# Optimization experiments

Hardware: AMD Instinct MI355X
Metric: run time of the kernel (lower is better)

Reference implementation:

```python
import jax, jax.numpy as jnp
import numpy as np
from jax import lax

NUM_PATHS = 16384
NUM_EDGES = 4096
LINK_DIM = 128   # link_state_dim (GRU input dim)
PATH_DIM = 128   # path_state_dim (GRU units)
MAX_LEN = 20     # max path length (static scatter shape)


def setup_inputs() -> dict:
    key = jax.random.key(0)
    ks = jax.random.split(key, 8)
    rng = np.random.default_rng(0)
    lens_np = rng.integers(4, MAX_LEN + 1, size=NUM_PATHS)
    lens_np[0] = MAX_LEN  # ensure max_len is reached
    total = int(lens_np.sum())
    idx_np = np.repeat(np.arange(NUM_PATHS), lens_np)
    offsets = np.repeat(np.concatenate([[0], np.cumsum(lens_np)[:-1]]), lens_np)
    seqs_np = np.arange(total) - offsets
    paths_np = rng.integers(0, NUM_EDGES, size=total)
    scale = 0.05
    return {
        "inputs": jax.random.normal(ks[0], (NUM_EDGES, LINK_DIM), jnp.float32),
        "paths": jnp.asarray(paths_np, jnp.int32),
        "idx": jnp.asarray(idx_np, jnp.int32),
        "seqs": jnp.asarray(seqs_np, jnp.int32),
        "lens": jnp.asarray(lens_np, jnp.int32),
        "gru_kernel": jax.random.normal(ks[1], (LINK_DIM, 3 * PATH_DIM), jnp.float32) * scale,
        "gru_rkernel": jax.random.normal(ks[2], (PATH_DIM, 3 * PATH_DIM), jnp.float32) * scale,
        "gru_bias": jax.random.normal(ks[3], (2, 3 * PATH_DIM), jnp.float32) * scale,
        "wq": jax.random.normal(ks[4], (PATH_DIM, PATH_DIM), jnp.float32) * scale,
        "wk": jax.random.normal(ks[5], (PATH_DIM, PATH_DIM), jnp.float32) * scale,
        "wv": jax.random.normal(ks[6], (PATH_DIM, PATH_DIM), jnp.float32) * scale,
    }


def _pem_forward(inputs, paths, idx, seqs, lens, gru_kernel, gru_rkernel, gru_bias, wq, wk, wv):
    P = lens.shape[0]
    D = gru_rkernel.shape[0]
    # gather per-step edge states and pack into padded [P, L, Din] sequences
    h_tild = inputs[paths]                                        # [T, Din]
    link_inputs = jnp.zeros((P, MAX_LEN, inputs.shape[1]), inputs.dtype)
    link_inputs = link_inputs.at[idx, seqs].set(h_tild)

    mask = jnp.arange(MAX_LEN, dtype=lens.dtype)[:, None] < lens[None, :]  # [L, P]
    xs = jnp.swapaxes(link_inputs, 0, 1)                          # [L, P, Din]

    def step(h, inp):
        x, m = inp
        xz, xr, xh = jnp.split(x @ gru_kernel + gru_bias[0], 3, axis=-1)
        hz, hr, hh = jnp.split(h @ gru_rkernel + gru_bias[1], 3, axis=-1)
        z = jax.nn.sigmoid(xz + hz)
        r = jax.nn.sigmoid(xr + hr)
        cand = jnp.tanh(xh + r * hh)
        h_new = z * h + (1.0 - z) * cand
        m2 = m[:, None]
        h_next = jnp.where(m2, h_new, h)        # carry state past sequence end
        y = jnp.where(m2, h_new, 0.0)           # zero outputs past sequence end
        return h_next, y

    h0 = jnp.zeros((P, D), inputs.dtype)
    last_state, hs = lax.scan(step, h0, (xs, mask))
    hidden_states = jnp.swapaxes(hs, 0, 1)                        # [P, L, D]

    key_ = jnp.einsum('pld,de->ple', hidden_states, wk)
    query = last_state @ wq                                       # [P, D]
    value = jnp.einsum('pld,de->ple', hidden_states, wv)
    att = jnp.einsum('pld,pd->pl', key_, query)                   # no softmax (as in source)
    context = jnp.einsum('pl,pld->pd', att, value)[:, None, :]    # [P, 1, D]
    return context


def reference(inputs, paths, idx, seqs, lens, gru_kernel, gru_rkernel, gru_bias, wq, wk, wv):
    return _pem_forward(inputs, paths, idx, seqs, lens,
                        gru_kernel, gru_rkernel, gru_bias, wq, wk, wv)
```

## Files before the change

### kernel.cpp

```cpp
#include <hip/hip_runtime.h>
#include <cstdint>

#define NP 16384
#define NE 4096
#define DIM 128
#define ML 20
#define TP 32
#define NT (NP/TP)

typedef _Float16 f16;
typedef _Float16 f16x8 __attribute__((ext_vector_type(8)));
typedef _Float16 f16x2 __attribute__((ext_vector_type(2)));
typedef float    f32x4 __attribute__((ext_vector_type(4)));

__global__ __launch_bounds__(1024) void k_sort(const int* __restrict__ lens,
                                               int* __restrict__ perm) {
    __shared__ int wcnt[16][33];
    __shared__ int start[ML + 1];
    const int tid = threadIdx.x;
    const int wv  = tid >> 6;
    for (int i = tid; i < 16 * 33; i += 1024) ((int*)wcnt)[i] = 0;
    __syncthreads();
    #pragma unroll
    for (int k = 0; k < NP / 1024; ++k) {
        const int p = k * 1024 + tid;
        atomicAdd(&wcnt[wv][lens[p]], 1);
    }
    __syncthreads();
    if (tid == 0) {
        int s = 0;
        for (int i = ML; i >= 0; --i) {
            int c = 0;
            #pragma unroll
            for (int w2 = 0; w2 < 16; ++w2) c += wcnt[w2][i];
            start[i] = s; s += c;
        }
    }
    __syncthreads();
    if (tid <= ML) {
        int running = start[tid];
        #pragma unroll
        for (int w2 = 0; w2 < 16; ++w2) {
            int tmp = wcnt[w2][tid];
            wcnt[w2][tid] = running;
            running += tmp;
        }
    }
    __syncthreads();
    #pragma unroll
    for (int k = 0; k < NP / 1024; ++k) {
        const int p = k * 1024 + tid;
        int pos = atomicAdd(&wcnt[wv][lens[p]], 1);
        perm[pos] = p;
    }
}

__global__ void k_prep(const int* __restrict__ idx, const int* __restrict__ seqs,
                       const int* __restrict__ paths, int total,
                       const float* __restrict__ inputs,
                       const float* __restrict__ gk, const float* __restrict__ gr,
                       int* __restrict__ edge_map, f16* __restrict__ inx,
                       f16* __restrict__ btz, f16* __restrict__ btr,
                       f16* __restrict__ btcx, f16* __restrict__ btch) {
    const int i = blockIdx.x * 256 + threadIdx.x;
    if (i < total) edge_map[idx[i] * ML + seqs[i]] = paths[i];
    inx[i] = (f16)inputs[i];
    if (i < 16384) {
        const int n = i >> 7, k = i & 127;
        btz[n*256 + k]       = (f16)gk[k*384 + n];
        btz[n*256 + 128 + k] = (f16)gr[k*384 + n];
        btr[n*256 + k]       = (f16)gk[k*384 + 128 + n];
        btr[n*256 + 128 + k] = (f16)gr[k*384 + 128 + n];
        btcx[n*128 + k]      = (f16)gk[k*384 + 256 + n];
        btch[n*128 + k]      = (f16)gr[k*384 + 256 + n];
    }
}

__device__ __forceinline__ float frcp(float x)  { return __builtin_amdgcn_rcpf(x); }
__device__ __forceinline__ float fsig(float x)  { return frcp(1.f + __expf(-x)); }
__device__ __forceinline__ float ftanh(float x) { float e = __expf(2.f * x); return 1.f - 2.f * frcp(e + 1.f); }


__global__ __launch_bounds__(512, 2) void k_gru(
    const f16* __restrict__ inx, const int* __restrict__ lens,
    const f16* __restrict__ btz, const f16* __restrict__ btr,
    const f16* __restrict__ btcx, const f16* __restrict__ btch,
    const float* __restrict__ gb, const int* __restrict__ edge_map,
    const int* __restrict__ perm, f16* __restrict__ hs, float* __restrict__ last)
{
    __shared__ f16 H16[2][TP * DIM];
    __shared__ int pgs[TP], lns[TP];

    const int tid  = threadIdx.x;
    const int lane = tid & 63;
    const int w    = tid >> 6;
    const int nw   = w * 16;
    const int arow = lane & 15;
    const int agrp = lane >> 4;
    const int d    = nw + arow;

    if (tid < TP) { int pg = perm[blockIdx.x * TP + tid]; pgs[tid] = pg; lns[tid] = lens[pg]; }
    for (int i = tid; i < TP * DIM; i += 512) H16[0][i] = (f16)0.f;
    asm volatile("s_waitcnt lgkmcnt(0)" ::: "memory");
    __builtin_amdgcn_s_barrier();

    int tmax = 0;
    #pragma unroll
    for (int i = 0; i < TP; ++i) tmax = max(tmax, lns[i]);

    f16x8 Bz[8], Br[8], Bx[4], Bh[4];
    {
        const int cb = d * 256 + agrp * 8;
        #pragma unroll
        for (int ks = 0; ks < 8; ++ks) {
            Bz[ks] = *(const f16x8*)(btz + cb + ks * 32);
            Br[ks] = *(const f16x8*)(btr + cb + ks * 32);
        }
        const int cc = d * 128 + agrp * 8;
        #pragma unroll
        for (int ks = 0; ks < 4; ++ks) {
            Bx[ks] = *(const f16x8*)(btcx + cc + ks * 32);
            Bh[ks] = *(const f16x8*)(btch + cc + ks * 32);
        }
    }

    const float bzc = gb[d]       + gb[384 + d];
    const float brc = gb[128 + d] + gb[512 + d];
    const float bxc = gb[256 + d];
    const float bhc = gb[640 + d];

    float hold0[4] = {0.f,0.f,0.f,0.f}, hold1[4] = {0.f,0.f,0.f,0.f};
    int ln0[4], ln1[4], hsr0[4], hsr1[4], h16a0[4], h16a1[4], pg0[4], pg1[4];
    #pragma unroll
    for (int r = 0; r < 4; ++r) {
        const int pa = agrp * 4 + r;
        const int pb = 16 + pa;
        ln0[r] = lns[pa];            ln1[r] = lns[pb];
        pg0[r] = pgs[pa];            pg1[r] = pgs[pb];
        hsr0[r] = pgs[pa] * ML;      hsr1[r] = pgs[pb] * ML;
        h16a0[r] = pa * DIM + (((d >> 3) ^ (pa & 7)) * 8) + (d & 7);
        h16a1[r] = pb * DIM + (((d >> 3) ^ (pb & 7)) * 8) + (d & 7);
    }

    const int ep0 = pgs[arow] * ML;
    const int ep1 = pgs[16 + arow] * ML;

    f16x8 xa0[4], xa1[4];
    int en0, en1;
    {
        const int e0 = edge_map[ep0] & (NE - 1);
        const int e1 = edge_map[ep1] & (NE - 1);
        const f16* xp0 = inx + e0 * DIM + agrp * 8;
        const f16* xp1 = inx + e1 * DIM + agrp * 8;
        #pragma unroll
        for (int ks = 0; ks < 4; ++ks) {
            xa0[ks] = *(const f16x8*)(xp0 + ks * 32);
            xa1[ks] = *(const f16x8*)(xp1 + ks * 32);
        }
        en0 = edge_map[ep0 + 1];
        en1 = edge_map[ep1 + 1];
    }

    for (int t = 0; t < tmax; ++t) {
        const f16* Hc = &H16[t & 1][0];
        f16*       Hn = &H16[(t & 1) ^ 1][0];

        f16x8 ha0[4], ha1[4];
        #pragma unroll
        for (int ks = 0; ks < 4; ++ks) {
            const int chunk = (ks * 4 + agrp) ^ (arow & 7);
            ha0[ks] = *(const f16x8*)(Hc + arow * DIM + chunk * 8);
            ha1[ks] = *(const f16x8*)(Hc + (16 + arow) * DIM + chunk * 8);
        }

        f32x4 Az0 = {0.f,0.f,0.f,0.f}, Ar0 = {0.f,0.f,0.f,0.f};
        f32x4 Ax0 = {0.f,0.f,0.f,0.f}, Ah0 = {0.f,0.f,0.f,0.f};
        f32x4 Az1 = {0.f,0.f,0.f,0.f}, Ar1 = {0.f,0.f,0.f,0.f};
        f32x4 Ax1 = {0.f,0.f,0.f,0.f}, Ah1 = {0.f,0.f,0.f,0.f};
        #pragma unroll
        for (int ks = 0; ks < 4; ++ks) {
            Az0 = __builtin_amdgcn_mfma_f32_16x16x32_f16(xa0[ks], Bz[ks], Az0, 0, 0, 0);
            Az1 = __builtin_amdgcn_mfma_f32_16x16x32_f16(xa1[ks], Bz[ks], Az1, 0, 0, 0);
            Ar0 = __builtin_amdgcn_mfma_f32_16x16x32_f16(xa0[ks], Br[ks], Ar0, 0, 0, 0);
            Ar1 = __builtin_amdgcn_mfma_f32_16x16x32_f16(xa1[ks], Br[ks], Ar1, 0, 0, 0);
            Ax0 = __builtin_amdgcn_mfma_f32_16x16x32_f16(xa0[ks], Bx[ks], Ax0, 0, 0, 0);
            Ax1 = __builtin_amdgcn_mfma_f32_16x16x32_f16(xa1[ks], Bx[ks], Ax1, 0, 0, 0);
        }
        #pragma unroll
        for (int ks = 0; ks < 4; ++ks) {
            Az0 = __builtin_amdgcn_mfma_f32_16x16x32_f16(ha0[ks], Bz[4 + ks], Az0, 0, 0, 0);
            Az1 = __builtin_amdgcn_mfma_f32_16x16x32_f16(ha1[ks], Bz[4 + ks], Az1, 0, 0, 0);
            Ar0 = __builtin_amdgcn_mfma_f32_16x16x32_f16(ha0[ks], Br[4 + ks], Ar0, 0, 0, 0);
            Ar1 = __builtin_amdgcn_mfma_f32_16x16x32_f16(ha1[ks], Br[4 + ks], Ar1, 0, 0, 0);
            Ah0 = __builtin_amdgcn_mfma_f32_16x16x32_f16(ha0[ks], Bh[ks],     Ah0, 0, 0, 0);
            Ah1 = __builtin_amdgcn_mfma_f32_16x16x32_f16(ha1[ks], Bh[ks],     Ah1, 0, 0, 0);
        }

        {
            const int e0 = en0 & (NE - 1);
            const int e1 = en1 & (NE - 1);
            const f16* xp0 = inx + e0 * DIM + agrp * 8;
            const f16* xp1 = inx + e1 * DIM + agrp * 8;
            #pragma unroll
            for (int ks = 0; ks < 4; ++ks) {
                xa0[ks] = *(const f16x8*)(xp0 + ks * 32);
                xa1[ks] = *(const f16x8*)(xp1 + ks * 32);
            }
            const int tn2 = (t + 2 < ML) ? (t + 2) : (ML - 1);
            en0 = edge_map[ep0 + tn2];
            en1 = edge_map[ep1 + tn2];
        }

        #pragma unroll
        for (int r = 0; r < 4; ++r) {
            const float z  = fsig(Az0[r] + bzc);
            const float rg = fsig(Ar0[r] + brc);
            const float c  = ftanh(Ax0[r] + bxc + rg * (Ah0[r] + bhc));
            const float hn = z * hold0[r] + (1.f - z) * c;
            hold0[r] = (t < ln0[r]) ? hn : hold0[r];
            const f16 hv = (f16)hold0[r];
            Hn[h16a0[r]] = hv;
            hs[(hsr0[r] + t) * DIM + d] = hv;
        }
        #pragma unroll
        for (int r = 0; r < 4; ++r) {
            const float z  = fsig(Az1[r] + bzc);
            const float rg = fsig(Ar1[r] + brc);
            const float c  = ftanh(Ax1[r] + bxc + rg * (Ah1[r] + bhc));
            const float hn = z * hold1[r] + (1.f - z) * c;
            hold1[r] = (t < ln1[r]) ? hn : hold1[r];
            const f16 hv = (f16)hold1[r];
            Hn[h16a1[r]] = hv;
            hs[(hsr1[r] + t) * DIM + d] = hv;
        }

        asm volatile("s_waitcnt lgkmcnt(0)" ::: "memory");
        __builtin_amdgcn_s_barrier();
    }

    #pragma unroll
    for (int r = 0; r < 4; ++r) {
        last[pg0[r] * DIM + d] = hold0[r];
        last[pg1[r] * DIM + d] = hold1[r];
    }
}


__global__ __launch_bounds__(256, 2) void k_qkq(
    const float* __restrict__ last, const float* __restrict__ wq,
    const float* __restrict__ wk, float* __restrict__ kq)
{
    __shared__ float LT[DIM][64];
    __shared__ float QT[DIM][64];
    const int tid = threadIdx.x;
    const int pb = blockIdx.x * 64;
    {
        const int p  = tid >> 2;
        const int dd = (tid & 3) * 32;
        const float4* src = (const float4*)(last + (pb + p) * DIM + dd);
        #pragma unroll
        for (int q = 0; q < 8; ++q) {
            float4 v = src[q];
            LT[dd + q * 4 + 0][p] = v.x; LT[dd + q * 4 + 1][p] = v.y;
            LT[dd + q * 4 + 2][p] = v.z; LT[dd + q * 4 + 3][p] = v.w;
        }
    }
    __syncthreads();
    const int e0 = (tid & 63) * 2;
    const int p0 = (tid >> 6) * 16;
    float a0[16], a1[16];
    #pragma unroll
    for (int i = 0; i < 16; ++i) { a0[i] = a1[i] = 0.f; }
    for (int dd = 0; dd < DIM; ++dd) {
        const float2 ww = *(const float2*)(wq + dd * DIM + e0);
        #pragma unroll
        for (int i = 0; i < 16; ++i) {
            const float lv = LT[dd][p0 + i];
            a0[i] = fmaf(lv, ww.x, a0[i]);
            a1[i] = fmaf(lv, ww.y, a1[i]);
        }
    }
    #pragma unroll
    for (int i = 0; i < 16; ++i) { QT[e0][p0 + i] = a0[i]; QT[e0 + 1][p0 + i] = a1[i]; }
    __syncthreads();
    float b0a[16], b1a[16];
    #pragma unroll
    for (int i = 0; i < 16; ++i) { b0a[i] = b1a[i] = 0.f; }
    for (int e = 0; e < DIM; ++e) {
        const float w0 = wk[e0 * DIM + e];
        const float w1 = wk[(e0 + 1) * DIM + e];
        #pragma unroll
        for (int i = 0; i < 16; ++i) {
            const float qv = QT[e][p0 + i];
            b0a[i] = fmaf(qv, w0, b0a[i]);
            b1a[i] = fmaf(qv, w1, b1a[i]);
        }
    }
    #pragma unroll
    for (int i = 0; i < 16; ++i) {
        float2 o; o.x = b0a[i]; o.y = b1a[i];
        *(float2*)(kq + (pb + p0 + i) * DIM + e0) = o;
    }
}


__global__ __launch_bounds__(256) void k_attn(
    const f16* __restrict__ hs, const float* __restrict__ kq,
    const int* __restrict__ lens, const float* __restrict__ wv,
    float* __restrict__ out)
{
    __shared__ float ctx[4][DIM];
    const int tid  = threadIdx.x;
    const int wave = tid >> 6;
    const int lane = tid & 63;
    const int p    = blockIdx.x * 4 + wave;
    const int ln   = lens[p];
    const float2 kqv = *(const float2*)(kq + p * DIM + lane * 2);
    float c0 = 0.f, c1 = 0.f;
    for (int l = 0; l < ln; ++l) {
        const f16x2 h2 = *(const f16x2*)(hs + (p * ML + l) * DIM + lane * 2);
        const float hx = (float)h2.x, hy = (float)h2.y;
        float s = hx * kqv.x + hy * kqv.y;
        #pragma unroll
        for (int off = 32; off > 0; off >>= 1) s += __shfl_xor(s, off, 64);
        c0 = fmaf(s, hx, c0);
        c1 = fmaf(s, hy, c1);
    }
    ctx[wave][lane * 2]     = c0;
    ctx[wave][lane * 2 + 1] = c1;
    __syncthreads();
    const int ee = lane * 2;
    float o0 = 0.f, o1 = 0.f;
    for (int dd = 0; dd < DIM; ++dd) {
        const float cv = ctx[wave][dd];
        const float2 ww = *(const float2*)(wv + dd * DIM + ee);
        o0 = fmaf(cv, ww.x, o0);
        o1 = fmaf(cv, ww.y, o1);
    }
    float2 o; o.x = o0; o.y = o1;
    *(float2*)(out + p * DIM + ee) = o;
}


extern "C" void kernel_launch(void* const* d_in, const int* in_sizes, int n_in,
                              void* d_out, int out_size, void* d_ws, size_t ws_size,
                              hipStream_t stream)
{
    const float* inputs = (const float*)d_in[0];
    const int*   paths  = (const int*)d_in[1];
    const int*   idx    = (const int*)d_in[2];
    const int*   seqs   = (const int*)d_in[3];
    const int*   lens   = (const int*)d_in[4];
    const float* gk     = (const float*)d_in[5];
    const float* gr     = (const float*)d_in[6];
    const float* gb     = (const float*)d_in[7];
    const float* wq     = (const float*)d_in[8];
    const float* wk     = (const float*)d_in[9];
    const float* wv     = (const float*)d_in[10];
    float* out = (float*)d_out;
    const int total = in_sizes[1];

    float* last = (float*)d_ws;
    float* kq   = last + (size_t)NP * DIM;
    f16*   hs   = (f16*)(kq + (size_t)NP * DIM);
    f16*   inx  = hs + (size_t)NP * ML * DIM;
    f16*   btz  = inx + (size_t)NE * DIM;
    f16*   btr  = btz + 128 * 256;
    f16*   btcx = btr + 128 * 256;
    f16*   btch = btcx + 128 * 128;
    int* edge_map = (int*)(btch + 128 * 128);
    int* perm   = edge_map + NP * ML;

    k_sort<<<1, 1024, 0, stream>>>(lens, perm);
    k_prep<<<(NE * DIM) / 256, 256, 0, stream>>>(idx, seqs, paths, total, inputs,
                                                 gk, gr, edge_map, inx,
                                                 btz, btr, btcx, btch);
    k_gru<<<NT, 512, 0, stream>>>(inx, lens, btz, btr, btcx, btch, gb, edge_map, perm, hs, last);
    k_qkq<<<NP / 64, 256, 0, stream>>>(last, wq, wk, kq);
    k_attn<<<NP / 4, 256, 0, stream>>>(hs, kq, lens, wv, out);
}
```

Before: 282.4 us.

## Fuse query/key projection into GRU kernel and software-pipeline input MFMAs

```diff
diff --git a/kernel.cpp b/kernel.cpp
--- a/kernel.cpp
+++ b/kernel.cpp
@@ -59,9 +59,11 @@
                        const int* __restrict__ paths, int total,
                        const float* __restrict__ inputs,
                        const float* __restrict__ gk, const float* __restrict__ gr,
+                       const float* __restrict__ wq, const float* __restrict__ wk,
                        int* __restrict__ edge_map, f16* __restrict__ inx,
                        f16* __restrict__ btz, f16* __restrict__ btr,
-                       f16* __restrict__ btcx, f16* __restrict__ btch) {
+                       f16* __restrict__ btcx, f16* __restrict__ btch,
+                       f16* __restrict__ wqt, f16* __restrict__ wkt) {
     const int i = blockIdx.x * 256 + threadIdx.x;
     if (i < total) edge_map[idx[i] * ML + seqs[i]] = paths[i];
     inx[i] = (f16)inputs[i];
@@ -73,6 +75,8 @@
         btr[n*256 + 128 + k] = (f16)gr[k*384 + 128 + n];
         btcx[n*128 + k]      = (f16)gk[k*384 + 256 + n];
         btch[n*128 + k]      = (f16)gr[k*384 + 256 + n];
+        wqt[n*128 + k]       = (f16)wq[k*128 + n];
+        wkt[n*128 + k]       = (f16)wk[n*128 + k];
     }
 }
 
@@ -85,8 +89,9 @@
     const f16* __restrict__ inx, const int* __restrict__ lens,
     const f16* __restrict__ btz, const f16* __restrict__ btr,
     const f16* __restrict__ btcx, const f16* __restrict__ btch,
+    const f16* __restrict__ wqt, const f16* __restrict__ wkt,
     const float* __restrict__ gb, const int* __restrict__ edge_map,
-    const int* __restrict__ perm, f16* __restrict__ hs, float* __restrict__ last)
+    const int* __restrict__ perm, f16* __restrict__ hs, float* __restrict__ kq)
 {
     __shared__ f16 H16[2][TP * DIM];
     __shared__ int pgs[TP], lns[TP];
@@ -145,6 +150,9 @@
     const int ep0 = pgs[arow] * ML;
     const int ep1 = pgs[16 + arow] * ML;
 
+    const f32x4 Z4 = {0.f, 0.f, 0.f, 0.f};
+    f32x4 Az0, Ar0, Ax0, Az1, Ar1, Ax1;
+
     f16x8 xa0[4], xa1[4];
     int en0, en1;
     {
@@ -159,24 +167,7 @@
         }
         en0 = edge_map[ep0 + 1];
         en1 = edge_map[ep1 + 1];
-    }
-
-    for (int t = 0; t < tmax; ++t) {
-        const f16* Hc = &H16[t & 1][0];
-        f16*       Hn = &H16[(t & 1) ^ 1][0];
-
-        f16x8 ha0[4], ha1[4];
-        #pragma unroll
-        for (int ks = 0; ks < 4; ++ks) {
-            const int chunk = (ks * 4 + agrp) ^ (arow & 7);
-            ha0[ks] = *(const f16x8*)(Hc + arow * DIM + chunk * 8);
-            ha1[ks] = *(const f16x8*)(Hc + (16 + arow) * DIM + chunk * 8);
-        }
-
-        f32x4 Az0 = {0.f,0.f,0.f,0.f}, Ar0 = {0.f,0.f,0.f,0.f};
-        f32x4 Ax0 = {0.f,0.f,0.f,0.f}, Ah0 = {0.f,0.f,0.f,0.f};
-        f32x4 Az1 = {0.f,0.f,0.f,0.f}, Ar1 = {0.f,0.f,0.f,0.f};
-        f32x4 Ax1 = {0.f,0.f,0.f,0.f}, Ah1 = {0.f,0.f,0.f,0.f};
+        Az0 = Z4; Ar0 = Z4; Ax0 = Z4; Az1 = Z4; Ar1 = Z4; Ax1 = Z4;
         #pragma unroll
         for (int ks = 0; ks < 4; ++ks) {
             Az0 = __builtin_amdgcn_mfma_f32_16x16x32_f16(xa0[ks], Bz[ks], Az0, 0, 0, 0);
@@ -186,6 +177,31 @@
             Ax0 = __builtin_amdgcn_mfma_f32_16x16x32_f16(xa0[ks], Bx[ks], Ax0, 0, 0, 0);
             Ax1 = __builtin_amdgcn_mfma_f32_16x16x32_f16(xa1[ks], Bx[ks], Ax1, 0, 0, 0);
         }
+        const int f0 = en0 & (NE - 1);
+        const int f1 = en1 & (NE - 1);
+        const f16* yp0 = inx + f0 * DIM + agrp * 8;
+        const f16* yp1 = inx + f1 * DIM + agrp * 8;
+        #pragma unroll
+        for (int ks = 0; ks < 4; ++ks) {
+            xa0[ks] = *(const f16x8*)(yp0 + ks * 32);
+            xa1[ks] = *(const f16x8*)(yp1 + ks * 32);
+        }
+        en0 = edge_map[ep0 + 2];
+        en1 = edge_map[ep1 + 2];
+    }
+
+    for (int t = 0; t < tmax; ++t) {
+        const f16* Hc = &H16[t & 1][0];
+        f16*       Hn = &H16[(t & 1) ^ 1][0];
+
+        f16x8 ha0[4], ha1[4];
+        #pragma unroll
+        for (int ks = 0; ks < 4; ++ks) {
+            const int chunk = (ks * 4 + agrp) ^ (arow & 7);
+            ha0[ks] = *(const f16x8*)(Hc + arow * DIM + chunk * 8);
+            ha1[ks] = *(const f16x8*)(Hc + (16 + arow) * DIM + chunk * 8);
+        }
+        f32x4 Ah0 = Z4, Ah1 = Z4;
         #pragma unroll
         for (int ks = 0; ks < 4; ++ks) {
             Az0 = __builtin_amdgcn_mfma_f32_16x16x32_f16(ha0[ks], Bz[4 + ks], Az0, 0, 0, 0);
@@ -196,6 +212,39 @@
             Ah1 = __builtin_amdgcn_mfma_f32_16x16x32_f16(ha1[ks], Bh[ks],     Ah1, 0, 0, 0);
         }
 
+        #pragma unroll
+        for (int r = 0; r < 4; ++r) {
+            const float z  = fsig(Az0[r] + bzc);
+            const float rg = fsig(Ar0[r] + brc);
+            const float c  = ftanh(Ax0[r] + bxc + rg * (Ah0[r] + bhc));
+            const float hn = z * hold0[r] + (1.f - z) * c;
+            hold0[r] = (t < ln0[r]) ? hn : hold0[r];
+            const f16 hv = (f16)hold0[r];
+            Hn[h16a0[r]] = hv;
+            hs[(hsr0[r] + t) * DIM + d] = hv;
+        }
+        #pragma unroll
+        for (int r = 0; r < 4; ++r) {
+            const float z  = fsig(Az1[r] + bzc);
+            const float rg = fsig(Ar1[r] + brc);
+            const float c  = ftanh(Ax1[r] + bxc + rg * (Ah1[r] + bhc));
+            const float hn = z * hold1[r] + (1.f - z) * c;
+            hold1[r] = (t < ln1[r]) ? hn : hold1[r];
+            const f16 hv = (f16)hold1[r];
+            Hn[h16a1[r]] = hv;
+            hs[(hsr1[r] + t) * DIM + d] = hv;
+        }
+
+        Az0 = Z4; Ar0 = Z4; Ax0 = Z4; Az1 = Z4; Ar1 = Z4; Ax1 = Z4;
+        #pragma unroll
+        for (int ks = 0; ks < 4; ++ks) {
+            Az0 = __builtin_amdgcn_mfma_f32_16x16x32_f16(xa0[ks], Bz[ks], Az0, 0, 0, 0);
+            Az1 = __builtin_amdgcn_mfma_f32_16x16x32_f16(xa1[ks], Bz[ks], Az1, 0, 0, 0);
+            Ar0 = __builtin_amdgcn_mfma_f32_16x16x32_f16(xa0[ks], Br[ks], Ar0, 0, 0, 0);
+            Ar1 = __builtin_amdgcn_mfma_f32_16x16x32_f16(xa1[ks], Br[ks], Ar1, 0, 0, 0);
+            Ax0 = __builtin_amdgcn_mfma_f32_16x16x32_f16(xa0[ks], Bx[ks], Ax0, 0, 0, 0);
+            Ax1 = __builtin_amdgcn_mfma_f32_16x16x32_f16(xa1[ks], Bx[ks], Ax1, 0, 0, 0);
+        }
         {
             const int e0 = en0 & (NE - 1);
             const int e1 = en1 & (NE - 1);
@@ -206,100 +255,66 @@
                 xa0[ks] = *(const f16x8*)(xp0 + ks * 32);
                 xa1[ks] = *(const f16x8*)(xp1 + ks * 32);
             }
-            const int tn2 = (t + 2 < ML) ? (t + 2) : (ML - 1);
-            en0 = edge_map[ep0 + tn2];
-            en1 = edge_map[ep1 + tn2];
-        }
-
-        #pragma unroll
-        for (int r = 0; r < 4; ++r) {
-            const float z  = fsig(Az0[r] + bzc);
-            const float rg = fsig(Ar0[r] + brc);
-            const float c  = ftanh(Ax0[r] + bxc + rg * (Ah0[r] + bhc));
-            const float hn = z * hold0[r] + (1.f - z) * c;
-            hold0[r] = (t < ln0[r]) ? hn : hold0[r];
-            const f16 hv = (f16)hold0[r];
-            Hn[h16a0[r]] = hv;
-            hs[(hsr0[r] + t) * DIM + d] = hv;
-        }
-        #pragma unroll
-        for (int r = 0; r < 4; ++r) {
-            const float z  = fsig(Az1[r] + bzc);
-            const float rg = fsig(Ar1[r] + brc);
-            const float c  = ftanh(Ax1[r] + bxc + rg * (Ah1[r] + bhc));
-            const float hn = z * hold1[r] + (1.f - z) * c;
-            hold1[r] = (t < ln1[r]) ? hn : hold1[r];
-            const f16 hv = (f16)hold1[r];
-            Hn[h16a1[r]] = hv;
-            hs[(hsr1[r] + t) * DIM + d] = hv;
+            const int tn3 = (t + 3 < ML) ? (t + 3) : (ML - 1);
+            en0 = edge_map[ep0 + tn3];
+            en1 = edge_map[ep1 + tn3];
         }
 
         asm volatile("s_waitcnt lgkmcnt(0)" ::: "memory");
         __builtin_amdgcn_s_barrier();
     }
 
-    #pragma unroll
-    for (int r = 0; r < 4; ++r) {
-        last[pg0[r] * DIM + d] = hold0[r];
-        last[pg1[r] * DIM + d] = hold1[r];
-    }
-}
-
-
-__global__ __launch_bounds__(256, 2) void k_qkq(
-    const float* __restrict__ last, const float* __restrict__ wq,
-    const float* __restrict__ wk, float* __restrict__ kq)
-{
-    __shared__ float LT[DIM][64];
-    __shared__ float QT[DIM][64];
-    const int tid = threadIdx.x;
-    const int pb = blockIdx.x * 64;
     {
-        const int p  = tid >> 2;
-        const int dd = (tid & 3) * 32;
-        const float4* src = (const float4*)(last + (pb + p) * DIM + dd);
-        #pragma unroll
-        for (int q = 0; q < 8; ++q) {
-            float4 v = src[q];
-            LT[dd + q * 4 + 0][p] = v.x; LT[dd + q * 4 + 1][p] = v.y;
-            LT[dd + q * 4 + 2][p] = v.z; LT[dd + q * 4 + 3][p] = v.w;
-        }
-    }
-    __syncthreads();
-    const int e0 = (tid & 63) * 2;
-    const int p0 = (tid >> 6) * 16;
-    float a0[16], a1[16];
-    #pragma unroll
-    for (int i = 0; i < 16; ++i) { a0[i] = a1[i] = 0.f; }
-    for (int dd = 0; dd < DIM; ++dd) {
-        const float2 ww = *(const float2*)(wq + dd * DIM + e0);
-        #pragma unroll
-        for (int i = 0; i < 16; ++i) {
-            const float lv = LT[dd][p0 + i];
-            a0[i] = fmaf(lv, ww.x, a0[i]);
-            a1[i] = fmaf(lv, ww.y, a1[i]);
-        }
-    }
-    #pragma unroll
-    for (int i = 0; i < 16; ++i) { QT[e0][p0 + i] = a0[i]; QT[e0 + 1][p0 + i] = a1[i]; }
-    __syncthreads();
-    float b0a[16], b1a[16];
-    #pragma unroll
-    for (int i = 0; i < 16; ++i) { b0a[i] = b1a[i] = 0.f; }
-    for (int e = 0; e < DIM; ++e) {
-        const float w0 = wk[e0 * DIM + e];
-        const float w1 = wk[(e0 + 1) * DIM + e];
-        #pragma unroll
-        for (int i = 0; i < 16; ++i) {
-            const float qv = QT[e][p0 + i];
-            b0a[i] = fmaf(qv, w0, b0a[i]);
-            b1a[i] = fmaf(qv, w1, b1a[i]);
-        }
-    }
-    #pragma unroll
-    for (int i = 0; i < 16; ++i) {
-        float2 o; o.x = b0a[i]; o.y = b1a[i];
-        *(float2*)(kq + (pb + p0 + i) * DIM + e0) = o;
+        const f16* Hf = &H16[tmax & 1][0];
+        f16*       Hq = &H16[(tmax & 1) ^ 1][0];
+
+        f16x8 Bq[4], Bk[4];
+        const int cw = d * 128 + agrp * 8;
+        #pragma unroll
+        for (int ks = 0; ks < 4; ++ks) {
+            Bq[ks] = *(const f16x8*)(wqt + cw + ks * 32);
+            Bk[ks] = *(const f16x8*)(wkt + cw + ks * 32);
+        }
+
+        f16x8 la0[4], la1[4];
+        #pragma unroll
+        for (int ks = 0; ks < 4; ++ks) {
+            const int chunk = (ks * 4 + agrp) ^ (arow & 7);
+            la0[ks] = *(const f16x8*)(Hf + arow * DIM + chunk * 8);
+            la1[ks] = *(const f16x8*)(Hf + (16 + arow) * DIM + chunk * 8);
+        }
+        f32x4 Aq0 = Z4, Aq1 = Z4;
+        #pragma unroll
+        for (int ks = 0; ks < 4; ++ks) {
+            Aq0 = __builtin_amdgcn_mfma_f32_16x16x32_f16(la0[ks], Bq[ks], Aq0, 0, 0, 0);
+            Aq1 = __builtin_amdgcn_mfma_f32_16x16x32_f16(la1[ks], Bq[ks], Aq1, 0, 0, 0);
+        }
+        #pragma unroll
+        for (int r = 0; r < 4; ++r) {
+            Hq[h16a0[r]] = (f16)Aq0[r];
+            Hq[h16a1[r]] = (f16)Aq1[r];
+        }
+        asm volatile("s_waitcnt lgkmcnt(0)" ::: "memory");
+        __builtin_amdgcn_s_barrier();
+
+        f16x8 qa0[4], qa1[4];
+        #pragma unroll
+        for (int ks = 0; ks < 4; ++ks) {
+            const int chunk = (ks * 4 + agrp) ^ (arow & 7);
+            qa0[ks] = *(const f16x8*)(Hq + arow * DIM + chunk * 8);
+            qa1[ks] = *(const f16x8*)(Hq + (16 + arow) * DIM + chunk * 8);
+        }
+        f32x4 Ak0 = Z4, Ak1 = Z4;
+        #pragma unroll
+        for (int ks = 0; ks < 4; ++ks) {
+            Ak0 = __builtin_amdgcn_mfma_f32_16x16x32_f16(qa0[ks], Bk[ks], Ak0, 0, 0, 0);
+            Ak1 = __builtin_amdgcn_mfma_f32_16x16x32_f16(qa1[ks], Bk[ks], Ak1, 0, 0, 0);
+        }
+        #pragma unroll
+        for (int r = 0; r < 4; ++r) {
+            kq[pg0[r] * DIM + d] = Ak0[r];
+            kq[pg1[r] * DIM + d] = Ak1[r];
+        }
     }
 }
 
@@ -360,22 +375,23 @@
     float* out = (float*)d_out;
     const int total = in_sizes[1];
 
-    float* last = (float*)d_ws;
-    float* kq   = last + (size_t)NP * DIM;
+    float* kq   = (float*)d_ws;
     f16*   hs   = (f16*)(kq + (size_t)NP * DIM);
     f16*   inx  = hs + (size_t)NP * ML * DIM;
     f16*   btz  = inx + (size_t)NE * DIM;
     f16*   btr  = btz + 128 * 256;
     f16*   btcx = btr + 128 * 256;
     f16*   btch = btcx + 128 * 128;
-    int* edge_map = (int*)(btch + 128 * 128);
+    f16*   wqt  = btch + 128 * 128;
+    f16*   wkt  = wqt + 128 * 128;
+    int* edge_map = (int*)(wkt + 128 * 128);
     int* perm   = edge_map + NP * ML;
 
     k_sort<<<1, 1024, 0, stream>>>(lens, perm);
     k_prep<<<(NE * DIM) / 256, 256, 0, stream>>>(idx, seqs, paths, total, inputs,
-                                                 gk, gr, edge_map, inx,
-                                                 btz, btr, btcx, btch);
-    k_gru<<<NT, 512, 0, stream>>>(inx, lens, btz, btr, btcx, btch, gb, edge_map, perm, hs, last);
-    k_qkq<<<NP / 64, 256, 0, stream>>>(last, wq, wk, kq);
+                                                 gk, gr, wq, wk, edge_map, inx,
+                                                 btz, btr, btcx, btch, wqt, wkt);
+    k_gru<<<NT, 512, 0, stream>>>(inx, lens, btz, btr, btcx, btch, wqt, wkt,
+                                  gb, edge_map, perm, hs, kq);
     k_attn<<<NP / 4, 256, 0, stream>>>(hs, kq, lens, wv, out);
 }
```

Result: faster. 268.5 us (-4.9%).
